# Performance work log

Measured on AMD Instinct MI355X. Metric: run time of the kernel, lower is better.

## Reference

```python
import jax, jax.numpy as jnp
import numpy as np

N = 50000      # nodes
E = 800000     # edges (avg degree 16)
D = 64         # in_feats
OUT = 64       # out_feats


def _xavier(key, shape, gain):
    fan_out, fan_in = shape
    limit = gain * np.sqrt(6.0 / (fan_in + fan_out))
    return jax.random.uniform(key, shape, jnp.float32, -limit, limit)


def setup_inputs() -> dict:
    key = jax.random.key(0)
    ks = jax.random.split(key, 8)
    gain = np.sqrt(2.0)  # calculate_gain('relu')
    feat = jax.random.normal(ks[0], (N, D), jnp.float32)
    weight = jax.random.uniform(ks[1], (E,), jnp.float32)
    src = jax.random.randint(ks[2], (E,), 0, N, jnp.int32)
    dst = jax.random.randint(ks[3], (E,), 0, N, jnp.int32)
    W_pool_src = _xavier(ks[4], (4 * D, D), gain)
    b_pool_src = jnp.zeros((4 * D,), jnp.float32)
    W_neigh = _xavier(ks[5], (OUT, 5 * D), gain)
    b_neigh = jnp.zeros((OUT,), jnp.float32)
    return {"feat": feat, "weight": weight, "src": src, "dst": dst,
            "W_pool_src": W_pool_src, "b_pool_src": b_pool_src,
            "W_neigh": W_neigh, "b_neigh": b_neigh}


def reference(feat, weight, src, dst, W_pool_src, b_pool_src, W_neigh, b_neigh):
    n = feat.shape[0]
    # fc_pool_src then split into the four per-stat feature blocks
    h = feat @ W_pool_src.T + b_pool_src                      # [N, 4D]
    h_sum, h_mean, h_max, h_std = jnp.split(h, 4, axis=-1)    # each [N, D]
    w = weight[:, None]                                       # [E, 1]

    deg = jax.ops.segment_sum(jnp.ones_like(weight), dst, num_segments=n)  # in-degrees [N]
    safe_deg = jnp.maximum(deg, 1.0)[:, None]

    # u_mul_e messages gathered at src, scattered to dst
    agg_sum = jax.ops.segment_sum(h_sum[src] * w, dst, num_segments=n)
    agg_mean = jax.ops.segment_sum(h_mean[src] * w, dst, num_segments=n) / safe_deg
    agg_max = jax.ops.segment_max(h_max[src] * w, dst, num_segments=n)
    m1 = jax.ops.segment_sum(h_std[src] * w, dst, num_segments=n) / safe_deg
    m2 = jax.ops.segment_sum((h_std * h_std)[src] * w, dst, num_segments=n) / safe_deg
    agg_std = m2 - m1 * m1                                    # neigh_std2 - neigh_std1**2

    h_neigh = jnp.concatenate([agg_sum, agg_mean, agg_max, agg_std], axis=-1)  # [N, 4D]
    h_neigh = jnp.where((deg == 0)[:, None], 0.0, h_neigh)    # zero isolated nodes

    rst = jnp.concatenate([feat, h_neigh], axis=-1) @ W_neigh.T + b_neigh      # [N, OUT]
    return rst
```

## Files before the change

kernel.cpp:

```cpp
#include <hip/hip_runtime.h>
#include <stdint.h>

#define NN 50000
#define NE 800000
#define NTILE16 3125
#define X2S 264
#define SCAP 128
#define LROW 64

typedef __attribute__((ext_vector_type(8))) short short8v;
typedef __attribute__((ext_vector_type(4))) float f32x4;

static __device__ __forceinline__ float bf2f(unsigned short u) {
    union { unsigned int i; float f; } v; v.i = ((unsigned int)u) << 16; return v.f;
}
static __device__ __forceinline__ unsigned short f2bf(float f) {
    union { float f; unsigned int i; } v; v.f = f;
    unsigned int x = v.i;
    x += 0x7fffu + ((x >> 16) & 1u);
    return (unsigned short)(x >> 16);
}
static __device__ __forceinline__ unsigned int pkbf(float lo, float hi) {
    return (unsigned int)f2bf(lo) | ((unsigned int)f2bf(hi) << 16);
}
static __device__ __forceinline__ unsigned int pk_edge(int src, float w) {
    union { _Float16 h; unsigned short u; } c; c.h = (_Float16)w;
    return (unsigned int)src | ((unsigned int)c.u << 16);
}
static __device__ __forceinline__ float edge_w(unsigned int ev) {
    union { unsigned short u; _Float16 h; } c; c.u = (unsigned short)(ev >> 16);
    return (float)c.h;
}

__global__ __launch_bounds__(256) void cvt_w_kernel(
    const float* __restrict__ Wp, const float* __restrict__ bp,
    const float* __restrict__ Wn,
    unsigned short* __restrict__ wnb2, unsigned short* __restrict__ wpb2,
    float* __restrict__ bpp2,
    float* __restrict__ uvec, float* __restrict__ vvec,
    int4* __restrict__ curzero)
{
    int i = blockIdx.x * 256 + threadIdx.x;
    if (i < 6250) curzero[i] = make_int4(0, 0, 0, 0);
    if (i < 20480) {
        int o = i / 320, k = i - o * 320;
        float val;
        if (k < 64) {
            val = Wn[o * 320 + k];
        } else if (k < 128) {
            int kk = k - 64; float s = 0.f;
            for (int c = 0; c < 64; ++c) s += Wn[o * 320 + 64 + c] * Wp[c * 64 + kk];
            val = s;
        } else if (k < 192) {
            int kk = k - 128; float s = 0.f;
            for (int c = 0; c < 64; ++c) s += Wn[o * 320 + 128 + c] * Wp[(64 + c) * 64 + kk];
            val = s;
        } else {
            val = Wn[o * 320 + k];
        }
        wnb2[i] = f2bf(val);
    } else if (i < 28672) {
        int idx = i - 20480;
        int j = idx >> 6, k = idx & 63;
        int r = (2 + (j & 1)) * 64 + (j >> 1);
        wpb2[idx] = f2bf(Wp[r * 64 + k]);
        if (k == 0) bpp2[j] = bp[r];
    } else if (i < 28800) {
        int j = i - 28672;
        if (j < 64) {
            float s = 0.f;
            for (int c = 0; c < 64; ++c) s += Wn[j * 320 + 64 + c] * bp[c];
            uvec[j] = s;
        } else {
            int o = j - 64; float s = 0.f;
            for (int c = 0; c < 64; ++c) s += Wn[o * 320 + 128 + c] * bp[64 + c];
            vvec[o] = s;
        }
    }
}

__global__ __launch_bounds__(256) void pool_mfma_kernel(
    const float* __restrict__ feat,
    const unsigned short* __restrict__ wpb2,
    const float* __restrict__ bpp2,
    unsigned short* __restrict__ featb,
    unsigned short* __restrict__ hpair)
{
    const int wave = threadIdx.x >> 6;
    const int lane = threadIdx.x & 63;
    const int tile = blockIdx.x * 4 + wave;
    if (tile >= NTILE16) return;
    const int n0 = tile * 16;
    const int nr = lane & 15;
    const int kq = (lane >> 4) * 8;
    const int node = n0 + nr;

    short8v bfrag[2];
    #pragma unroll
    for (int s = 0; s < 2; ++s) {
        const float4* fp = (const float4*)(feat + (size_t)node * 64 + s * 32 + kq);
        float4 a = fp[0], b = fp[1];
        union { unsigned int u[4]; short8v v; uint4 q; } au;
        au.u[0] = pkbf(a.x, a.y); au.u[1] = pkbf(a.z, a.w);
        au.u[2] = pkbf(b.x, b.y); au.u[3] = pkbf(b.z, b.w);
        bfrag[s] = au.v;
        *(uint4*)(featb + (size_t)node * 64 + s * 32 + kq) = au.q;
    }

    f32x4 acc[8];
    #pragma unroll
    for (int t = 0; t < 8; ++t) acc[t] = (f32x4){0.f, 0.f, 0.f, 0.f};

    #pragma unroll
    for (int t = 0; t < 8; ++t) {
        #pragma unroll
        for (int s = 0; s < 2; ++s) {
            short8v a = *(const short8v*)(wpb2 + (size_t)(t * 16 + nr) * 64 + s * 32 + kq);
            acc[t] = __builtin_amdgcn_mfma_f32_16x16x32_bf16(a, bfrag[s], acc[t], 0, 0, 0);
        }
    }

    const int csub = (lane >> 4) * 4;
    #pragma unroll
    for (int t = 0; t < 8; ++t) {
        const int c0 = t * 8 + (lane >> 4) * 2;
        const float4 bb = *(const float4*)(bpp2 + t * 16 + csub);
        const float hm0 = acc[t][0] + bb.x, hs0 = acc[t][1] + bb.y;
        const float hm1 = acc[t][2] + bb.z, hs1 = acc[t][3] + bb.w;
        int pk = __builtin_amdgcn_cvt_pk_fp8_f32(hm0, hs0, 0, false);
        pk = __builtin_amdgcn_cvt_pk_fp8_f32(hm1, hs1, pk, true);
        *(unsigned int*)((char*)hpair + (size_t)node * 128 + c0 * 2) = (unsigned int)pk;
    }
}

__global__ __launch_bounds__(256) void bin_kernel(
    const int* __restrict__ srcE, const int* __restrict__ dstE,
    const float* __restrict__ wE,
    int* __restrict__ bcur,
    uint2* __restrict__ bucket)
{
    const int gtid = blockIdx.x * 256 + threadIdx.x;
    const int sub = blockIdx.x & 7;
    if (gtid < NE / 4) {
        int4 s4 = ((const int4*)srcE)[gtid];
        int4 d4 = ((const int4*)dstE)[gtid];
        float4 w4 = ((const float4*)wE)[gtid];
        int b0 = (d4.x >> 4) * 8 + sub, l0 = d4.x & 15;
        int b1 = (d4.y >> 4) * 8 + sub, l1 = d4.y & 15;
        int b2 = (d4.z >> 4) * 8 + sub, l2 = d4.z & 15;
        int b3 = (d4.w >> 4) * 8 + sub, l3 = d4.w & 15;
        int p0 = atomicAdd(&bcur[b0], 1);
        int p1 = atomicAdd(&bcur[b1], 1);
        int p2 = atomicAdd(&bcur[b2], 1);
        int p3 = atomicAdd(&bcur[b3], 1);
        if (p0 < SCAP) bucket[(size_t)b0 * SCAP + p0] = make_uint2(pk_edge(s4.x, w4.x), l0);
        if (p1 < SCAP) bucket[(size_t)b1 * SCAP + p1] = make_uint2(pk_edge(s4.y, w4.y), l1);
        if (p2 < SCAP) bucket[(size_t)b2 * SCAP + p2] = make_uint2(pk_edge(s4.z, w4.z), l2);
        if (p3 < SCAP) bucket[(size_t)b3 * SCAP + p3] = make_uint2(pk_edge(s4.w, w4.w), l3);
    }
}

__global__ __launch_bounds__(512) void fused_gather_epi_kernel(
    const unsigned short* __restrict__ featb,
    const unsigned short* __restrict__ hpair,
    const int* __restrict__ bcur,
    const uint2* __restrict__ bucket,
    const unsigned short* __restrict__ wnb2,
    const float* __restrict__ bn,
    const float* __restrict__ uvec,
    const float* __restrict__ vvec,
    float* __restrict__ out)
{
    __shared__ unsigned int ldsCSR[16 * LROW];
    __shared__ int ldsCnt[16];
    __shared__ unsigned short x2[16 * X2S];
    __shared__ float swl[16], invl[16];

    const int tid  = threadIdx.x;
    const int wave = tid >> 6;
    const int lane = tid & 63;
    const int n0 = blockIdx.x * 16;

    if (tid < 16) ldsCnt[tid] = 0;
    __syncthreads();
    const int bb = blockIdx.x * 8;
    #pragma unroll
    for (int sub = 0; sub < 8; ++sub) {
        const int scnt = min(bcur[bb + sub], SCAP);
        const uint2* bp = bucket + (size_t)(bb + sub) * SCAP;
        for (int i = tid; i < scnt; i += 512) {
            uint2 e = bp[i];
            int loc = (int)e.y;
            int p = atomicAdd(&ldsCnt[loc], 1);
            if (p < LROW) ldsCSR[loc * LROW + p] = e.x;
        }
    }
    __syncthreads();

    #pragma unroll
    for (int nb = 0; nb < 2; ++nb) {
        const int node = wave * 2 + nb;
        const int dg = min(ldsCnt[node], LROW);
        float g1 = 0.f, vmx = -INFINITY, s2 = 0.f, s3 = 0.f, sw = 0.f;

        {
            const int cnt = dg;
            unsigned int ewv = 0;
            if (lane < cnt) ewv = ldsCSR[node * LROW + lane];
            const int cm1 = cnt - 1;
            for (int jj = 0; jj < cnt; jj += 8) {
                unsigned short fv[8]; unsigned short hv[8]; unsigned int ev[8];
                #pragma unroll
                for (int u = 0; u < 8; ++u) {
                    int ic = min(jj + u, cm1);
                    ev[u] = __builtin_amdgcn_readlane(ewv, ic);
                    int sj = ev[u] & 0xFFFFu;
                    fv[u] = featb[(size_t)sj * 64 + lane];
                    hv[u] = hpair[(size_t)sj * 64 + lane];
                }
                #pragma unroll
                for (int u = 0; u < 8; ++u) {
                    bool valid = (jj + u) < cnt;
                    float wr = edge_w(ev[u]);
                    float wj = valid ? wr : 0.f;
                    float f  = bf2f(fv[u]);
                    int hvi  = (int)hv[u];
                    float hm = __builtin_amdgcn_cvt_f32_fp8(hvi, 0);
                    float hs = __builtin_amdgcn_cvt_f32_fp8(hvi, 1);
                    g1 = fmaf(wj, f, g1);
                    float m = valid ? wj * hm : -INFINITY;
                    vmx = fmaxf(vmx, m);
                    s3 = fmaf(wj, hs, s3);
                    s2 = fmaf(wj * hs, hs, s2);
                    sw += wj;
                }
            }
        }

        const float inv = 1.0f / (float)max(dg, 1);
        const float m1 = s3 * inv;
        const float astd = (dg > 0) ? (s2 * inv - m1 * m1) : 0.f;
        unsigned short* row = x2 + node * X2S;
        row[lane]       = f2bf(g1);
        row[64 + lane]  = f2bf(g1 * inv);
        row[128 + lane] = f2bf(dg > 0 ? vmx : 0.f);
        row[192 + lane] = f2bf(astd);
        if (lane == 0) { swl[node] = sw; invl[node] = inv; }
    }
    __syncthreads();

    if (wave >= 4) return;
    const int nr = lane & 15;
    const int kq = (lane >> 4) * 8;
    const int col = wave * 16 + nr;
    const int orow = (lane >> 4) * 4;

    f32x4 acc = (f32x4){0.f, 0.f, 0.f, 0.f};
    #pragma unroll
    for (int s = 0; s < 2; ++s) {
        short8v a = *(const short8v*)(featb + (size_t)(n0 + nr) * 64 + s * 32 + kq);
        short8v b = *(const short8v*)(wnb2 + (size_t)col * 320 + s * 32 + kq);
        acc = __builtin_amdgcn_mfma_f32_16x16x32_bf16(a, b, acc, 0, 0, 0);
    }
    #pragma unroll
    for (int s = 2; s < 10; ++s) {
        short8v a = *(const short8v*)(x2 + nr * X2S + (s - 2) * 32 + kq);
        short8v b = *(const short8v*)(wnb2 + (size_t)col * 320 + s * 32 + kq);
        acc = __builtin_amdgcn_mfma_f32_16x16x32_bf16(a, b, acc, 0, 0, 0);
    }

    const float bb2 = bn[col], uu = uvec[col], vv = vvec[col];
    #pragma unroll
    for (int i = 0; i < 4; ++i) {
        const int node = orow + i;
        const float o = acc[i] + bb2 + swl[node] * uu + swl[node] * invl[node] * vv;
        out[(size_t)(n0 + node) * 64 + col] = o;
    }
}

extern "C" void kernel_launch(void* const* d_in, const int* in_sizes, int n_in,
                              void* d_out, int out_size, void* d_ws, size_t ws_size,
                              hipStream_t stream)
{
    const float* feat   = (const float*)d_in[0];
    const float* weight = (const float*)d_in[1];
    const int*   src    = (const int*)d_in[2];
    const int*   dst    = (const int*)d_in[3];
    const float* Wp     = (const float*)d_in[4];
    const float* bp     = (const float*)d_in[5];
    const float* Wn     = (const float*)d_in[6];
    const float* bn     = (const float*)d_in[7];
    float* out = (float*)d_out;

    char* ws = (char*)d_ws;
    size_t cur0 = 0;
    auto alloc = [&](size_t bytes) -> void* {
        cur0 = (cur0 + 255) & ~(size_t)255;
        void* p = ws + cur0;
        cur0 += bytes;
        return p;
    };

    unsigned short* hpair = (unsigned short*)alloc((size_t)NN * 64 * 2);
    int* bcur            = (int*)alloc((size_t)NTILE16 * 8 * 4);
    uint2* bucket        = (uint2*)alloc((size_t)NTILE16 * 8 * SCAP * 8);
    unsigned short* featb= (unsigned short*)alloc((size_t)NN * 64 * 2);
    unsigned short* wnb2 = (unsigned short*)alloc((size_t)64 * 320 * 2);
    unsigned short* wpb2 = (unsigned short*)alloc((size_t)128 * 64 * 2);
    float* bpp2          = (float*)alloc((size_t)128 * 4);
    float* uvec          = (float*)alloc((size_t)64 * 4);
    float* vvec          = (float*)alloc((size_t)64 * 4);
    (void)ws_size; (void)in_sizes; (void)n_in; (void)out_size;

    cvt_w_kernel<<<129, 256, 0, stream>>>(Wp, bp, Wn, wnb2, wpb2, bpp2, uvec, vvec,
                                          (int4*)bcur);
    pool_mfma_kernel<<<(NTILE16 + 3) / 4, 256, 0, stream>>>(feat, wpb2, bpp2,
                                                            featb, hpair);
    bin_kernel<<<(NE / 4 + 255) / 256, 256, 0, stream>>>(src, dst, weight, bcur, bucket);
    fused_gather_epi_kernel<<<NTILE16, 512, 0, stream>>>(featb, hpair, bcur, bucket,
                                                         wnb2, bn, uvec, vvec, out);
}
```

Measured before the change: 132.7 us.

## Fuse edge binning into pool kernel with per-node sub-bucket CSR

Removes the separate edge-binning kernel and moves edge scattering into the pool MFMA kernel, whose grid is enlarged so each block bins 256 edges. Bins change from 16-node tile buckets to per-(sub, node) cells of 16 slots, spreading atomics over many more counters to reduce contention. The gather kernel now loads fixed-size uint4 chunks per cell instead of looping over variable-length buckets. The trade-off is a much larger, sparse workspace that must be zeroed and read back, plus a hard cap of 16 edges per node per sub-bin that would silently drop edges on overflow.

New measurement: 120.3 us. -9.3%, faster.

```diff
diff --git a/kernel.cpp b/kernel.cpp
--- a/kernel.cpp
+++ b/kernel.cpp
@@ -5,7 +5,8 @@
 #define NE 800000
 #define NTILE16 3125
 #define X2S 264
-#define SCAP 128
+#define NSUB 8
+#define SUBCAP 16
 #define LROW 64
 
 typedef __attribute__((ext_vector_type(8))) short short8v;
@@ -41,7 +42,7 @@
     int4* __restrict__ curzero)
 {
     int i = blockIdx.x * 256 + threadIdx.x;
-    if (i < 6250) curzero[i] = make_int4(0, 0, 0, 0);
+    if (i < 100000) curzero[i] = make_int4(0, 0, 0, 0);
     if (i < 20480) {
         int o = i / 320, k = i - o * 320;
         float val;
@@ -81,11 +82,26 @@
 
 __global__ __launch_bounds__(256) void pool_mfma_kernel(
     const float* __restrict__ feat,
+    const int* __restrict__ srcE,
+    const int* __restrict__ dstE,
+    const float* __restrict__ wE,
+    int* __restrict__ cur8,
+    unsigned int* __restrict__ csr8,
     const unsigned short* __restrict__ wpb2,
     const float* __restrict__ bpp2,
     unsigned short* __restrict__ featb,
     unsigned short* __restrict__ hpair)
 {
+    {
+        const int e = blockIdx.x * 256 + threadIdx.x;
+        const int sub = blockIdx.x & 7;
+        int d = dstE[e];
+        int cell = sub * NN + d;
+        int r = atomicAdd(&cur8[cell], 1);
+        if (r < SUBCAP)
+            csr8[((size_t)cell << 4) + r] = pk_edge(srcE[e], wE[e]);
+    }
+
     const int wave = threadIdx.x >> 6;
     const int lane = threadIdx.x & 63;
     const int tile = blockIdx.x * 4 + wave;
@@ -133,38 +149,11 @@
     }
 }
 
-__global__ __launch_bounds__(256) void bin_kernel(
-    const int* __restrict__ srcE, const int* __restrict__ dstE,
-    const float* __restrict__ wE,
-    int* __restrict__ bcur,
-    uint2* __restrict__ bucket)
-{
-    const int gtid = blockIdx.x * 256 + threadIdx.x;
-    const int sub = blockIdx.x & 7;
-    if (gtid < NE / 4) {
-        int4 s4 = ((const int4*)srcE)[gtid];
-        int4 d4 = ((const int4*)dstE)[gtid];
-        float4 w4 = ((const float4*)wE)[gtid];
-        int b0 = (d4.x >> 4) * 8 + sub, l0 = d4.x & 15;
-        int b1 = (d4.y >> 4) * 8 + sub, l1 = d4.y & 15;
-        int b2 = (d4.z >> 4) * 8 + sub, l2 = d4.z & 15;
-        int b3 = (d4.w >> 4) * 8 + sub, l3 = d4.w & 15;
-        int p0 = atomicAdd(&bcur[b0], 1);
-        int p1 = atomicAdd(&bcur[b1], 1);
-        int p2 = atomicAdd(&bcur[b2], 1);
-        int p3 = atomicAdd(&bcur[b3], 1);
-        if (p0 < SCAP) bucket[(size_t)b0 * SCAP + p0] = make_uint2(pk_edge(s4.x, w4.x), l0);
-        if (p1 < SCAP) bucket[(size_t)b1 * SCAP + p1] = make_uint2(pk_edge(s4.y, w4.y), l1);
-        if (p2 < SCAP) bucket[(size_t)b2 * SCAP + p2] = make_uint2(pk_edge(s4.z, w4.z), l2);
-        if (p3 < SCAP) bucket[(size_t)b3 * SCAP + p3] = make_uint2(pk_edge(s4.w, w4.w), l3);
-    }
-}
-
 __global__ __launch_bounds__(512) void fused_gather_epi_kernel(
     const unsigned short* __restrict__ featb,
     const unsigned short* __restrict__ hpair,
-    const int* __restrict__ bcur,
-    const uint2* __restrict__ bucket,
+    const int* __restrict__ cur8,
+    const unsigned int* __restrict__ csr8,
     const unsigned short* __restrict__ wnb2,
     const float* __restrict__ bn,
     const float* __restrict__ uvec,
@@ -183,16 +172,22 @@
 
     if (tid < 16) ldsCnt[tid] = 0;
     __syncthreads();
-    const int bb = blockIdx.x * 8;
-    #pragma unroll
-    for (int sub = 0; sub < 8; ++sub) {
-        const int scnt = min(bcur[bb + sub], SCAP);
-        const uint2* bp = bucket + (size_t)(bb + sub) * SCAP;
-        for (int i = tid; i < scnt; i += 512) {
-            uint2 e = bp[i];
-            int loc = (int)e.y;
-            int p = atomicAdd(&ldsCnt[loc], 1);
-            if (p < LROW) ldsCSR[loc * LROW + p] = e.x;
+    {
+        const int row  = tid >> 2;
+        const int part = tid & 3;
+        const int sub  = row >> 4;
+        const int node = row & 15;
+        const int cell = sub * NN + (n0 + node);
+        const int cnt  = min(cur8[cell], SUBCAP);
+        const uint4 e4 = ((const uint4*)(csr8 + ((size_t)cell << 4)))[part];
+        const int base = part * 4;
+        unsigned int vals[4] = {e4.x, e4.y, e4.z, e4.w};
+        #pragma unroll
+        for (int j = 0; j < 4; ++j) {
+            if (base + j < cnt) {
+                int p = atomicAdd(&ldsCnt[node], 1);
+                if (p < LROW) ldsCSR[node * LROW + p] = vals[j];
+            }
         }
     }
     __syncthreads();
@@ -269,11 +264,11 @@
         acc = __builtin_amdgcn_mfma_f32_16x16x32_bf16(a, b, acc, 0, 0, 0);
     }
 
-    const float bb2 = bn[col], uu = uvec[col], vv = vvec[col];
+    const float bb = bn[col], uu = uvec[col], vv = vvec[col];
     #pragma unroll
     for (int i = 0; i < 4; ++i) {
         const int node = orow + i;
-        const float o = acc[i] + bb2 + swl[node] * uu + swl[node] * invl[node] * vv;
+        const float o = acc[i] + bb + swl[node] * uu + swl[node] * invl[node] * vv;
         out[(size_t)(n0 + node) * 64 + col] = o;
     }
 }
@@ -302,8 +297,8 @@
     };
 
     unsigned short* hpair = (unsigned short*)alloc((size_t)NN * 64 * 2);
-    int* bcur            = (int*)alloc((size_t)NTILE16 * 8 * 4);
-    uint2* bucket        = (uint2*)alloc((size_t)NTILE16 * 8 * SCAP * 8);
+    int* cur8            = (int*)alloc((size_t)NSUB * NN * 4);
+    unsigned int* csr8   = (unsigned int*)alloc((size_t)NSUB * NN * SUBCAP * 4);
     unsigned short* featb= (unsigned short*)alloc((size_t)NN * 64 * 2);
     unsigned short* wnb2 = (unsigned short*)alloc((size_t)64 * 320 * 2);
     unsigned short* wpb2 = (unsigned short*)alloc((size_t)128 * 64 * 2);
@@ -312,11 +307,11 @@
     float* vvec          = (float*)alloc((size_t)64 * 4);
     (void)ws_size; (void)in_sizes; (void)n_in; (void)out_size;
 
-    cvt_w_kernel<<<129, 256, 0, stream>>>(Wp, bp, Wn, wnb2, wpb2, bpp2, uvec, vvec,
-                                          (int4*)bcur);
-    pool_mfma_kernel<<<(NTILE16 + 3) / 4, 256, 0, stream>>>(feat, wpb2, bpp2,
-                                                            featb, hpair);
-    bin_kernel<<<(NE / 4 + 255) / 256, 256, 0, stream>>>(src, dst, weight, bcur, bucket);
-    fused_gather_epi_kernel<<<NTILE16, 512, 0, stream>>>(featb, hpair, bcur, bucket,
+    cvt_w_kernel<<<391, 256, 0, stream>>>(Wp, bp, Wn, wnb2, wpb2, bpp2, uvec, vvec,
+                                          (int4*)cur8);
+    pool_mfma_kernel<<<NTILE16, 256, 0, stream>>>(feat, src, dst, weight,
+                                                  cur8, csr8, wpb2, bpp2,
+                                                  featb, hpair);
+    fused_gather_epi_kernel<<<NTILE16, 512, 0, stream>>>(featb, hpair, cur8, csr8,
                                                          wnb2, bn, uvec, vvec, out);
 }
```
